# Kernel tuning notes

Measured on AMD Instinct MI355X. Metric: run time of the kernel, lower is better.

## Reference

```python
import itertools
import jax, jax.numpy as jnp
import numpy as np

N = 400000
CIN, COUT = 32, 64
K, STRIDE, PAD, DIL = 3, 2, 1, 1
SPATIAL = (200, 200, 16)
PRUNING_RATIO = 0.5

def _out_spatial():
    return tuple((s + 2 * PAD - DIL * (K - 1) - 1) // STRIDE + 1 for s in SPATIAL)


def setup_inputs() -> dict:
    key = jax.random.key(0)
    kf, kc0, kc1, kc2, kc3, km, kw = jax.random.split(key, 7)
    features = jax.random.normal(kf, (N, CIN), dtype=jnp.float32)
    b = jax.random.randint(kc0, (N,), 0, 2, dtype=jnp.int32)
    z = jax.random.randint(kc1, (N,), 0, SPATIAL[0], dtype=jnp.int32)
    y = jax.random.randint(kc2, (N,), 0, SPATIAL[1], dtype=jnp.int32)
    x = jax.random.randint(kc3, (N,), 0, SPATIAL[2], dtype=jnp.int32)
    coors = jnp.stack([b, z, y, x], axis=1)  # [N,4] = (batch, d0, d1, d2)
    mask = jax.random.uniform(km, (N,), dtype=jnp.float32)
    weight = jax.random.normal(kw, (K, K, K, CIN, COUT), dtype=jnp.float32) * 0.05
    return {"features": features, "coors": coors, "mask": mask, "weight": weight, "batch_size": 2}


def _sprs_conv(features, coors, mask, weight, batch_size):
    out_sp = _out_spatial()  # (100, 100, 8)
    num_out = batch_size * out_sp[0] * out_sp[1] * out_sp[2]
    n = features.shape[0]
    # rank-based pruning: keep top (1 - pruning_ratio) points as 'important'
    thr = jnp.sort(mask)[int(n * PRUNING_RATIO)]
    important = (mask >= thr)  # [N] bool

    b = coors[:, 0]
    pos = coors[:, 1:4]  # [N,3]
    out_sp_arr = jnp.array(out_sp, dtype=pos.dtype)

    # accumulators; slot num_out is a dump for invalid indices
    acc = jnp.zeros((num_out + 1, COUT), dtype=features.dtype)
    imp_cnt = jnp.zeros((num_out + 1,), dtype=jnp.int32)

    for off in itertools.product(range(K), repeat=3):
        off_arr = jnp.array(off, dtype=pos.dtype)
        num = pos + PAD - DIL * off_arr  # [N,3]
        oc = num // STRIDE
        valid = jnp.all(num % STRIDE == 0, axis=-1) & jnp.all(oc >= 0, axis=-1) & jnp.all(oc < out_sp_arr, axis=-1)
        lin = ((b * out_sp[0] + oc[:, 0]) * out_sp[1] + oc[:, 1]) * out_sp[2] + oc[:, 2]
        idx = jnp.where(valid, lin, num_out)
        vals = features @ weight[off[0], off[1], off[2]]  # [N,Cout] gather-GEMM
        acc = acc.at[idx].add(vals)  # scatter
        imp_cnt = imp_cnt.at[idx].add((important & valid).astype(jnp.int32))

    keep = (imp_cnt[:num_out] > 0)  # output positions reached by >=1 important point
    return acc[:num_out] * keep[:, None]


def reference(features, coors, mask, weight, batch_size):
    return _sprs_conv(features, coors, mask, weight, batch_size)
```

## Files before the change

kernel.cpp:

```cpp
#include <hip/hip_runtime.h>

#define CIN 32
#define COUT 64
#define OD0 100
#define OD1 100
#define OD2 8
#define IZ 200
#define IY 200
#define IX 16
#define NTAP 27
#define NCELLS (2 * IZ * IY * IX)
#define TOY 4
#define TOX 8
#define NROW 27
#define NCELL_R (NROW * 16)
#define CAPB 384


__global__ void hist0_fused_kernel(const float* __restrict__ mask, const int* __restrict__ coors,
                                   const float* __restrict__ W, int n,
                                   int* __restrict__ hist, int* __restrict__ S,
                                   float* __restrict__ Wt) {
    __shared__ int h[256];
    h[threadIdx.x] = 0;
    __syncthreads();
    for (int i = blockIdx.x * blockDim.x + threadIdx.x; i < n; i += gridDim.x * blockDim.x) {
        unsigned bits = __float_as_uint(mask[i]);
        atomicAdd(&h[bits >> 24], 1);
        const int4 c = ((const int4*)coors)[i];
        atomicAdd(&S[((c.x * IZ + c.y) * IY + c.z) * IX + c.w], 1);
    }
    for (int i = blockIdx.x * blockDim.x + threadIdx.x; i < NTAP * CIN * COUT;
         i += gridDim.x * blockDim.x) {
        int cout = i % COUT;
        int rest = i / COUT;
        int cin = rest % CIN;
        int tap = rest / CIN;
        Wt[((size_t)tap * COUT + cout) * CIN + cin] = W[i];
    }
    __syncthreads();
    int v = h[threadIdx.x];
    if (v) atomicAdd(&hist[threadIdx.x], v);
}


__global__ void hist8_kernel(const float* __restrict__ mask, int n, int level,
                             const int* __restrict__ state, int* __restrict__ hist) {
    __shared__ int h[256];
    h[threadIdx.x] = 0;
    __syncthreads();
    unsigned pfx = (unsigned)state[0];
    int sh = 24 - 8 * level;
    for (int i = blockIdx.x * blockDim.x + threadIdx.x; i < n; i += gridDim.x * blockDim.x) {
        unsigned bits = __float_as_uint(mask[i]);
        if ((bits >> (sh + 8)) == pfx)
            atomicAdd(&h[(bits >> sh) & 0xFF], 1);
    }
    __syncthreads();
    int v = h[threadIdx.x];
    if (v) atomicAdd(&hist[threadIdx.x], v);
}

__global__ void select8_kernel(const int* __restrict__ hist, int* __restrict__ state,
                               int level, int rankConst) {
    __shared__ int sc[256];
    sc[threadIdx.x] = hist[threadIdx.x];
    __syncthreads();
    if (threadIdx.x == 0) {
        int rank = level ? state[1] : rankConst;
        unsigned pfx = level ? (unsigned)state[0] : 0u;
        int c = 0;
        for (int j = 0; j < 256; j++) {
            int hv = sc[j];
            if (rank < c + hv) {
                state[0] = (int)((pfx << 8) | (unsigned)j);
                state[1] = rank - c;
                break;
            }
            c += hv;
        }
    }
}


__global__ void scan_l0_kernel(int* __restrict__ S, int* __restrict__ partials) {
    __shared__ int ts[256];
    int tid = threadIdx.x;
    int4 v = ((int4*)S)[blockIdx.x * 256 + tid];
    int s1 = v.x + v.y, s2 = s1 + v.z, s3 = s2 + v.w;
    ts[tid] = s3;
    __syncthreads();
    for (int off = 1; off < 256; off <<= 1) {
        int t = (tid >= off) ? ts[tid - off] : 0;
        __syncthreads();
        ts[tid] += t;
        __syncthreads();
    }
    int excl = ts[tid] - s3;
    int4 o;
    o.x = excl; o.y = excl + v.x; o.z = excl + s1; o.w = excl + s2;
    ((int4*)S)[blockIdx.x * 256 + tid] = o;
    if (tid == 255) partials[blockIdx.x] = ts[255];
}

__global__ void scan_l1_kernel(int* __restrict__ partials, int nP) {
    __shared__ int sums[256];
    int tid = threadIdx.x;
    int per = (nP + 255) / 256;
    int lo = tid * per, hi = lo + per;
    if (hi > nP) hi = nP;
    int s = 0;
    for (int j = lo; j < hi; j++) s += partials[j];
    sums[tid] = s;
    __syncthreads();
    for (int off = 1; off < 256; off <<= 1) {
        int t = (tid >= off) ? sums[tid - off] : 0;
        __syncthreads();
        sums[tid] += t;
        __syncthreads();
    }
    int run = sums[tid] - s;
    for (int j = lo; j < hi; j++) { int v = partials[j]; partials[j] = run; run += v; }
}

__global__ void scan_l2_kernel(int* __restrict__ S, const int* __restrict__ partials) {
    int add = partials[blockIdx.x];
    if (add == 0) return;
    int4 v = ((int4*)S)[blockIdx.x * 256 + threadIdx.x];
    v.x += add; v.y += add; v.z += add; v.w += add;
    ((int4*)S)[blockIdx.x * 256 + threadIdx.x] = v;
}

__global__ void scatter_points_kernel(const int* __restrict__ coors, const float* __restrict__ mask,
                                      const int* __restrict__ state, int n,
                                      int* __restrict__ S, int* __restrict__ entries) {
    int i = blockIdx.x * blockDim.x + threadIdx.x;
    if (i >= n) return;
    const int4 c = ((const int4*)coors)[i];
    int cell = ((c.x * IZ + c.y) * IY + c.z) * IX + c.w;
    float thr = __uint_as_float((unsigned)state[0]);
    int imp = (mask[i] >= thr) ? 1 : 0;
    int pos = atomicAdd(&S[cell], 1);
    entries[pos] = (i << 1) | imp;
}


__global__ void __launch_bounds__(256)
conv_kernel(const float* __restrict__ feat, const float* __restrict__ Wt,
            const int* __restrict__ S, const int* __restrict__ entries,
            float* __restrict__ out) {
    __shared__ float accS[TOY * TOX][COUT];
    __shared__ int   keepS[TOY * TOX];
    __shared__ int   sLds[NROW][17];
    __shared__ unsigned work[6][CAPB];
    __shared__ int   cnt[6];
    __shared__ int   notDone;

    int tid = threadIdx.x;
    int w = tid >> 6;
    int lane = tid & 63;

    int tile = blockIdx.x;
    int oyT = (tile % (OD1 / TOY)) * TOY;
    int rest = tile / (OD1 / TOY);
    int oz = rest % OD0;
    int bb = rest / OD0;

    {
        float4 z = make_float4(0.f, 0.f, 0.f, 0.f);
        float4* a4 = (float4*)&accS[0][0];
        a4[tid] = z;
        a4[tid + 256] = z;
        if (tid < TOY * TOX) keepS[tid] = 0;
    }

    for (int idx = tid; idx < NROW * 17; idx += 256) {
        int row = idx / 17, j = idx % 17;
        int plane = row / 9, pyL = row % 9;
        int pz = 2 * oz - 1 + plane;
        int py = 2 * oyT - 1 + pyL;
        int v = 0;
        if (pz >= 0 && py >= 0) {
            int cellFlat = ((bb * IZ + pz) * IY + py) * IX + (j - 1);
            if (cellFlat >= 0) v = S[cellFlat];
        }
        sLds[row][j] = v;
    }
    __syncthreads();

    int myCl[2]; int nMy = 0;
    for (int cl = tid; cl < NCELL_R; cl += 256) myCl[nMy++] = cl;
    int ci = 0;
    int pi = -1;

    for (;;) {
        if (tid < 6) cnt[tid] = 0;
        if (tid == 0) notDone = 0;
        __syncthreads();

        while (ci < nMy) {
            int cl = myCl[ci];
            int row = cl >> 4, px = cl & 15;
            int rs = (pi < 0) ? sLds[row][px] : pi;
            int re = sLds[row][px + 1];
            int plane = row / 9, pyL = row % 9;
            int bin = plane * 2 + (pyL & 1);
            bool blocked = false;
            for (int i = rs; i < re; i++) {
                int pos = atomicAdd(&cnt[bin], 1);
                if (pos >= CAPB) { pi = i; blocked = true; break; }
                int e = entries[i];
                work[bin][pos] = ((unsigned)(e >> 1) << 9) | (unsigned)((e & 1) << 8)
                               | (unsigned)(pyL << 4) | (unsigned)px;
            }
            if (blocked) break;
            ci++; pi = -1;
        }
        if (ci < nMy) notDone = 1;
        __syncthreads();

        for (int t = w; t < NTAP; t += 4) {
            int o0 = t / 9, r9 = t % 9, o1 = r9 / 3, o2 = r9 % 3;
            int bin = o0 * 2 + (o1 & 1);
            int nb = cnt[bin];
            if (nb > CAPB) nb = CAPB;
            if (nb == 0) continue;

            const float4* wp = (const float4*)(Wt + ((size_t)t * COUT + lane) * CIN);
            float4 w0 = wp[0], w1 = wp[1], w2 = wp[2], w3 = wp[3];
            float4 w4 = wp[4], w5 = wp[5], w6 = wp[6], w7 = wp[7];

            int pcl = -1;
            float4 f0, f1, f2, f3, f4, f5, f6, f7;

            for (int j = 0; j < nb; j++) {
                unsigned e = work[bin][j];
                int pyL = (int)((e >> 4) & 15u);
                int px  = (int)(e & 15u);
                int yy = (pyL - o1) >> 1;
                if ((unsigned)yy >= (unsigned)TOY) continue;
                int dx = px + 1 - o2;
                if (dx & 1) continue;
                int ox = dx >> 1;
                if ((unsigned)ox >= (unsigned)TOX) continue;

                int pid = (int)(e >> 9);
                const float4* fp = (const float4*)(feat + (size_t)pid * CIN);
                float4 n0 = fp[0], n1 = fp[1], n2 = fp[2], n3 = fp[3];
                float4 n4 = fp[4], n5 = fp[5], n6 = fp[6], n7 = fp[7];

                if (pcl >= 0) {
                    float a0 = 0.f, a1 = 0.f, a2 = 0.f, a3 = 0.f;
                    a0 = fmaf(f0.x, w0.x, a0); a0 = fmaf(f0.y, w0.y, a0);
                    a0 = fmaf(f0.z, w0.z, a0); a0 = fmaf(f0.w, w0.w, a0);
                    a1 = fmaf(f1.x, w1.x, a1); a1 = fmaf(f1.y, w1.y, a1);
                    a1 = fmaf(f1.z, w1.z, a1); a1 = fmaf(f1.w, w1.w, a1);
                    a2 = fmaf(f2.x, w2.x, a2); a2 = fmaf(f2.y, w2.y, a2);
                    a2 = fmaf(f2.z, w2.z, a2); a2 = fmaf(f2.w, w2.w, a2);
                    a3 = fmaf(f3.x, w3.x, a3); a3 = fmaf(f3.y, w3.y, a3);
                    a3 = fmaf(f3.z, w3.z, a3); a3 = fmaf(f3.w, w3.w, a3);
                    a0 = fmaf(f4.x, w4.x, a0); a0 = fmaf(f4.y, w4.y, a0);
                    a0 = fmaf(f4.z, w4.z, a0); a0 = fmaf(f4.w, w4.w, a0);
                    a1 = fmaf(f5.x, w5.x, a1); a1 = fmaf(f5.y, w5.y, a1);
                    a1 = fmaf(f5.z, w5.z, a1); a1 = fmaf(f5.w, w5.w, a1);
                    a2 = fmaf(f6.x, w6.x, a2); a2 = fmaf(f6.y, w6.y, a2);
                    a2 = fmaf(f6.z, w6.z, a2); a2 = fmaf(f6.w, w6.w, a2);
                    a3 = fmaf(f7.x, w7.x, a3); a3 = fmaf(f7.y, w7.y, a3);
                    a3 = fmaf(f7.z, w7.z, a3); a3 = fmaf(f7.w, w7.w, a3);
                    atomicAdd(&accS[pcl][lane], (a0 + a1) + (a2 + a3));
                }

                f0 = n0; f1 = n1; f2 = n2; f3 = n3;
                f4 = n4; f5 = n5; f6 = n6; f7 = n7;
                pcl = yy * TOX + ox;
                if (lane == 0 && (e & 0x100u)) keepS[pcl] = 1;
            }

            if (pcl >= 0) {
                float a0 = 0.f, a1 = 0.f, a2 = 0.f, a3 = 0.f;
                a0 = fmaf(f0.x, w0.x, a0); a0 = fmaf(f0.y, w0.y, a0);
                a0 = fmaf(f0.z, w0.z, a0); a0 = fmaf(f0.w, w0.w, a0);
                a1 = fmaf(f1.x, w1.x, a1); a1 = fmaf(f1.y, w1.y, a1);
                a1 = fmaf(f1.z, w1.z, a1); a1 = fmaf(f1.w, w1.w, a1);
                a2 = fmaf(f2.x, w2.x, a2); a2 = fmaf(f2.y, w2.y, a2);
                a2 = fmaf(f2.z, w2.z, a2); a2 = fmaf(f2.w, w2.w, a2);
                a3 = fmaf(f3.x, w3.x, a3); a3 = fmaf(f3.y, w3.y, a3);
                a3 = fmaf(f3.z, w3.z, a3); a3 = fmaf(f3.w, w3.w, a3);
                a0 = fmaf(f4.x, w4.x, a0); a0 = fmaf(f4.y, w4.y, a0);
                a0 = fmaf(f4.z, w4.z, a0); a0 = fmaf(f4.w, w4.w, a0);
                a1 = fmaf(f5.x, w5.x, a1); a1 = fmaf(f5.y, w5.y, a1);
                a1 = fmaf(f5.z, w5.z, a1); a1 = fmaf(f5.w, w5.w, a1);
                a2 = fmaf(f6.x, w6.x, a2); a2 = fmaf(f6.y, w6.y, a2);
                a2 = fmaf(f6.z, w6.z, a2); a2 = fmaf(f6.w, w6.w, a2);
                a3 = fmaf(f7.x, w7.x, a3); a3 = fmaf(f7.y, w7.y, a3);
                a3 = fmaf(f7.z, w7.z, a3); a3 = fmaf(f7.w, w7.w, a3);
                atomicAdd(&accS[pcl][lane], (a0 + a1) + (a2 + a3));
            }
        }
        __syncthreads();
        if (!notDone) break;
    }

#pragma unroll
    for (int k = 0; k < 8; k++) {
        int cl = w * 8 + k;
        int oy = oyT + (cl >> 3);
        int ox = cl & 7;
        size_t cellG = (((size_t)bb * OD0 + oz) * OD1 + oy) * OD2 + ox;
        out[cellG * COUT + lane] = keepS[cl] ? accS[cl][lane] : 0.f;
    }
}


__global__ void hist0_simple_kernel(const float* __restrict__ mask, int n, int* __restrict__ hist) {
    __shared__ int h[256];
    h[threadIdx.x] = 0;
    __syncthreads();
    for (int i = blockIdx.x * blockDim.x + threadIdx.x; i < n; i += gridDim.x * blockDim.x) {
        unsigned bits = __float_as_uint(mask[i]);
        atomicAdd(&h[bits >> 24], 1);
    }
    __syncthreads();
    int v = h[threadIdx.x];
    if (v) atomicAdd(&hist[threadIdx.x], v);
}

__global__ void __launch_bounds__(256)
scatter_kernel(const float* __restrict__ feat, const int* __restrict__ coors,
               const float* __restrict__ mask, const float* __restrict__ W,
               const int* __restrict__ state, float* __restrict__ out,
               int* __restrict__ keep, int n) {
    int gid = blockIdx.x * blockDim.x + threadIdx.x;
    int wave = gid >> 6;
    int lane = threadIdx.x & 63;
    if (wave >= n) return;

    const int4 c4 = ((const int4*)coors)[wave];
    int bb = c4.x, pz = c4.y, py = c4.z, px = c4.w;

    float thr = __uint_as_float((unsigned)state[0]);
    bool imp = mask[wave] >= thr;

    int oz[2], ozo[2], nz = 0;
    int oy[2], oyo[2], ny = 0;
    int ox[2], oxo[2], nx = 0;
#pragma unroll
    for (int o = 0; o < 3; o++) {
        int num = pz + 1 - o;
        if (num >= 0 && !(num & 1) && (num >> 1) < OD0) { oz[nz] = num >> 1; ozo[nz] = o; nz++; }
        num = py + 1 - o;
        if (num >= 0 && !(num & 1) && (num >> 1) < OD1) { oy[ny] = num >> 1; oyo[ny] = o; ny++; }
        num = px + 1 - o;
        if (num >= 0 && !(num & 1) && (num >> 1) < OD2) { ox[nx] = num >> 1; oxo[nx] = o; nx++; }
    }

    float f[CIN];
    const float4* fp = (const float4*)(feat + (size_t)wave * CIN);
#pragma unroll
    for (int j = 0; j < CIN / 4; j++) {
        float4 v = fp[j];
        f[4 * j + 0] = v.x; f[4 * j + 1] = v.y; f[4 * j + 2] = v.z; f[4 * j + 3] = v.w;
    }

    for (int a = 0; a < nz; a++)
        for (int b = 0; b < ny; b++)
            for (int c = 0; c < nx; c++) {
                int woff = ((ozo[a] * 3 + oyo[b]) * 3 + oxo[c]) * (CIN * COUT);
                const float* wcol = W + woff + lane;
                float acc = 0.f;
#pragma unroll
                for (int k = 0; k < CIN; k++) acc = fmaf(f[k], wcol[k * COUT], acc);
                int lin = ((bb * OD0 + oz[a]) * OD1 + oy[b]) * OD2 + ox[c];
                atomicAdd(out + (size_t)lin * COUT + lane, acc);
                if (imp && lane == 0) keep[lin] = 1;
            }
}

__global__ void finalize_kernel(float* __restrict__ out, const int* __restrict__ keep, int numOut) {
    int t = blockIdx.x * blockDim.x + threadIdx.x;
    if (t >= numOut * (COUT / 4)) return;
    int o = t >> 4;
    if (!keep[o]) ((float4*)out)[t] = make_float4(0.f, 0.f, 0.f, 0.f);
}


extern "C" void kernel_launch(void* const* d_in, const int* in_sizes, int n_in,
                              void* d_out, int out_size, void* d_ws, size_t ws_size,
                              hipStream_t stream) {
    const float* feat  = (const float*)d_in[0];
    const int*   coors = (const int*)d_in[1];
    const float* mask  = (const float*)d_in[2];
    const float* W     = (const float*)d_in[3];

    int n = in_sizes[2];
    int numOut = out_size / COUT;
    int rank = (int)(n * 0.5);

    const int blk = 256;
    int gN = (n + blk - 1) / blk;

    char* ws = (char*)d_ws;

    size_t offHist    = 0;
    size_t offState   = 4 * 256 * 4;
    size_t offS       = offState + 64;
    size_t offPart    = offS + (size_t)NCELLS * 4;
    size_t offEntries = offPart + 1280 * 4;
    size_t offWt      = offEntries + (size_t)n * 4;
    size_t need       = offWt + (size_t)NTAP * CIN * COUT * 4;

    int* hist  = (int*)(ws + offHist);
    int* state = (int*)(ws + offState);

    if (ws_size >= need) {
        int*   S       = (int*)(ws + offS);
        int*   part    = (int*)(ws + offPart);
        int*   entries = (int*)(ws + offEntries);
        float* Wt      = (float*)(ws + offWt);

        hipMemsetAsync(ws, 0, offS + (size_t)NCELLS * 4, stream);

        hist0_fused_kernel<<<256, blk, 0, stream>>>(mask, coors, W, n, hist, S, Wt);
        select8_kernel<<<1, 256, 0, stream>>>(hist, state, 0, rank);
        for (int lvl = 1; lvl < 4; lvl++) {
            hist8_kernel<<<256, blk, 0, stream>>>(mask, n, lvl, state, hist + lvl * 256);
            select8_kernel<<<1, 256, 0, stream>>>(hist + lvl * 256, state, lvl, rank);
        }

        int nBlocksScan = NCELLS / 1024;
        scan_l0_kernel<<<nBlocksScan, 256, 0, stream>>>(S, part);
        scan_l1_kernel<<<1, 256, 0, stream>>>(part, nBlocksScan);
        scan_l2_kernel<<<nBlocksScan, 256, 0, stream>>>(S, part);
        scatter_points_kernel<<<gN, blk, 0, stream>>>(coors, mask, state, n, S, entries);

        int nTiles = numOut / (TOY * TOX);
        conv_kernel<<<nTiles, 256, 0, stream>>>(feat, Wt, S, entries, (float*)d_out);
    } else {
        int* keep = (int*)(ws + offS);
        hipMemsetAsync(d_out, 0, (size_t)out_size * sizeof(float), stream);
        hipMemsetAsync(ws, 0, offS + (size_t)numOut * 4, stream);

        hist0_simple_kernel<<<256, blk, 0, stream>>>(mask, n, hist);
        select8_kernel<<<1, 256, 0, stream>>>(hist, state, 0, rank);
        for (int lvl = 1; lvl < 4; lvl++) {
            hist8_kernel<<<256, blk, 0, stream>>>(mask, n, lvl, state, hist + lvl * 256);
            select8_kernel<<<1, 256, 0, stream>>>(hist + lvl * 256, state, lvl, rank);
        }

        long long threads = (long long)n * 64;
        int gScatter = (int)((threads + blk - 1) / blk);
        scatter_kernel<<<gScatter, blk, 0, stream>>>(feat, coors, mask, W, state,
                                                     (float*)d_out, keep, n);

        int fin = numOut * (COUT / 4);
        finalize_kernel<<<(fin + blk - 1) / blk, blk, 0, stream>>>((float*)d_out, keep, numOut);
    }
}
```

Baseline: 733.6 us.

## Use two-pass 16-bit radix select and widen conv blocks to 512 threads

The top-k threshold search drops from four 8-bit histogram and select rounds to two 16-bit rounds, which removes several small serial kernel launches. The first histogram now goes straight to global atomics on a 65536-bin table instead of a shared-memory histogram. Separately, the conv kernel runs with 512 threads (8 waves) per tile, so each thread loads at most one cell and taps are spread over 8 waves, with an extra barrier to compute the done flag. Global atomic contention in the high histogram and a larger memset may offset the savings.

```diff
diff --git a/kernel.cpp b/kernel.cpp
--- a/kernel.cpp
+++ b/kernel.cpp
@@ -19,14 +19,11 @@
 
 __global__ void hist0_fused_kernel(const float* __restrict__ mask, const int* __restrict__ coors,
                                    const float* __restrict__ W, int n,
-                                   int* __restrict__ hist, int* __restrict__ S,
+                                   int* __restrict__ histHi, int* __restrict__ S,
                                    float* __restrict__ Wt) {
-    __shared__ int h[256];
-    h[threadIdx.x] = 0;
-    __syncthreads();
     for (int i = blockIdx.x * blockDim.x + threadIdx.x; i < n; i += gridDim.x * blockDim.x) {
         unsigned bits = __float_as_uint(mask[i]);
-        atomicAdd(&h[bits >> 24], 1);
+        atomicAdd(&histHi[bits >> 16], 1);
         const int4 c = ((const int4*)coors)[i];
         atomicAdd(&S[((c.x * IZ + c.y) * IY + c.z) * IX + c.w], 1);
     }
@@ -38,43 +35,74 @@
         int tap = rest / CIN;
         Wt[((size_t)tap * COUT + cout) * CIN + cin] = W[i];
     }
-    __syncthreads();
-    int v = h[threadIdx.x];
-    if (v) atomicAdd(&hist[threadIdx.x], v);
-}
-
-
-__global__ void hist8_kernel(const float* __restrict__ mask, int n, int level,
-                             const int* __restrict__ state, int* __restrict__ hist) {
-    __shared__ int h[256];
-    h[threadIdx.x] = 0;
-    __syncthreads();
-    unsigned pfx = (unsigned)state[0];
-    int sh = 24 - 8 * level;
-    for (int i = blockIdx.x * blockDim.x + threadIdx.x; i < n; i += gridDim.x * blockDim.x) {
-        unsigned bits = __float_as_uint(mask[i]);
-        if ((bits >> (sh + 8)) == pfx)
-            atomicAdd(&h[(bits >> sh) & 0xFF], 1);
-    }
-    __syncthreads();
-    int v = h[threadIdx.x];
-    if (v) atomicAdd(&hist[threadIdx.x], v);
-}
-
-__global__ void select8_kernel(const int* __restrict__ hist, int* __restrict__ state,
-                               int level, int rankConst) {
-    __shared__ int sc[256];
-    sc[threadIdx.x] = hist[threadIdx.x];
-    __syncthreads();
-    if (threadIdx.x == 0) {
-        int rank = level ? state[1] : rankConst;
-        unsigned pfx = level ? (unsigned)state[0] : 0u;
+}
+
+__global__ void hist_hi_simple_kernel(const float* __restrict__ mask, int n, int* __restrict__ hist) {
+    int i = blockIdx.x * blockDim.x + threadIdx.x;
+    if (i >= n) return;
+    unsigned bits = __float_as_uint(mask[i]);
+    atomicAdd(&hist[bits >> 16], 1);
+}
+
+__global__ void select16_kernel(const int* __restrict__ hist, const int* rankSrc,
+                                int rankConst, int* __restrict__ outPair) {
+    __shared__ int partial[256];
+    __shared__ int scan[257];
+    int t = threadIdx.x;
+    int rank = rankSrc ? *rankSrc : rankConst;
+    const int* h = hist + t * 256;
+    int sum = 0;
+    for (int j = 0; j < 256; j++) sum += h[j];
+    partial[t] = sum;
+    __syncthreads();
+    if (t == 0) {
         int c = 0;
+        for (int j = 0; j < 256; j++) { scan[j] = c; c += partial[j]; }
+        scan[256] = c;
+    }
+    __syncthreads();
+    int base = scan[t];
+    if (rank >= base && rank < scan[t + 1]) {
+        int c = base;
         for (int j = 0; j < 256; j++) {
-            int hv = sc[j];
+            int hv = h[j];
+            if (rank < c + hv) { outPair[0] = t * 256 + j; outPair[1] = rank - c; break; }
+            c += hv;
+        }
+    }
+}
+
+__global__ void hist_lo_kernel(const float* __restrict__ mask, int n,
+                               const int* __restrict__ state, int* __restrict__ hist) {
+    int i = blockIdx.x * blockDim.x + threadIdx.x;
+    if (i >= n) return;
+    unsigned bits = __float_as_uint(mask[i]);
+    if ((int)(bits >> 16) == state[2]) atomicAdd(&hist[bits & 0xFFFFu], 1);
+}
+
+__global__ void selectLo_kernel(const int* __restrict__ hist, int* __restrict__ state) {
+    __shared__ int partial[256];
+    __shared__ int scan[257];
+    int t = threadIdx.x;
+    int rank = state[3];
+    const int* h = hist + t * 256;
+    int sum = 0;
+    for (int j = 0; j < 256; j++) sum += h[j];
+    partial[t] = sum;
+    __syncthreads();
+    if (t == 0) {
+        int c = 0;
+        for (int j = 0; j < 256; j++) { scan[j] = c; c += partial[j]; }
+        scan[256] = c;
+    }
+    __syncthreads();
+    int base = scan[t];
+    if (rank >= base && rank < scan[t + 1]) {
+        int c = base;
+        for (int j = 0; j < 256; j++) {
+            int hv = h[j];
             if (rank < c + hv) {
-                state[0] = (int)((pfx << 8) | (unsigned)j);
-                state[1] = rank - c;
+                state[0] = (state[2] << 16) | (t * 256 + j);
                 break;
             }
             c += hv;
@@ -145,7 +173,7 @@
 }
 
 
-__global__ void __launch_bounds__(256)
+__global__ void __launch_bounds__(512, 6)
 conv_kernel(const float* __restrict__ feat, const float* __restrict__ Wt,
             const int* __restrict__ S, const int* __restrict__ entries,
             float* __restrict__ out) {
@@ -168,13 +196,11 @@
 
     {
         float4 z = make_float4(0.f, 0.f, 0.f, 0.f);
-        float4* a4 = (float4*)&accS[0][0];
-        a4[tid] = z;
-        a4[tid + 256] = z;
+        ((float4*)&accS[0][0])[tid] = z;
         if (tid < TOY * TOX) keepS[tid] = 0;
     }
 
-    for (int idx = tid; idx < NROW * 17; idx += 256) {
+    for (int idx = tid; idx < NROW * 17; idx += 512) {
         int row = idx / 17, j = idx % 17;
         int plane = row / 9, pyL = row % 9;
         int pz = 2 * oz - 1 + plane;
@@ -188,9 +214,7 @@
     }
     __syncthreads();
 
-    int myCl[2]; int nMy = 0;
-    for (int cl = tid; cl < NCELL_R; cl += 256) myCl[nMy++] = cl;
-    int ci = 0;
+    int myCell = (tid < NCELL_R) ? tid : -1;
     int pi = -1;
 
     for (;;) {
@@ -198,9 +222,8 @@
         if (tid == 0) notDone = 0;
         __syncthreads();
 
-        while (ci < nMy) {
-            int cl = myCl[ci];
-            int row = cl >> 4, px = cl & 15;
+        if (myCell >= 0) {
+            int row = myCell >> 4, px = myCell & 15;
             int rs = (pi < 0) ? sLds[row][px] : pi;
             int re = sLds[row][px + 1];
             int plane = row / 9, pyL = row % 9;
@@ -213,13 +236,16 @@
                 work[bin][pos] = ((unsigned)(e >> 1) << 9) | (unsigned)((e & 1) << 8)
                                | (unsigned)(pyL << 4) | (unsigned)px;
             }
-            if (blocked) break;
-            ci++; pi = -1;
+            if (!blocked) myCell = -1;
         }
-        if (ci < nMy) notDone = 1;
-        __syncthreads();
-
-        for (int t = w; t < NTAP; t += 4) {
+        __syncthreads();
+        if (tid == 0) notDone = 0;
+        __syncthreads();
+        if (myCell >= 0) notDone = 1;
+        __syncthreads();
+        int more = notDone;
+
+        for (int t = w; t < NTAP; t += 8) {
             int o0 = t / 9, r9 = t % 9, o1 = r9 / 3, o2 = r9 % 3;
             int bin = o0 * 2 + (o1 & 1);
             int nb = cnt[bin];
@@ -298,12 +324,12 @@
             }
         }
         __syncthreads();
-        if (!notDone) break;
+        if (!more) break;
     }
 
 #pragma unroll
-    for (int k = 0; k < 8; k++) {
-        int cl = w * 8 + k;
+    for (int k = 0; k < 4; k++) {
+        int cl = w * 4 + k;
         int oy = oyT + (cl >> 3);
         int ox = cl & 7;
         size_t cellG = (((size_t)bb * OD0 + oz) * OD1 + oy) * OD2 + ox;
@@ -311,19 +337,6 @@
     }
 }
 
-
-__global__ void hist0_simple_kernel(const float* __restrict__ mask, int n, int* __restrict__ hist) {
-    __shared__ int h[256];
-    h[threadIdx.x] = 0;
-    __syncthreads();
-    for (int i = blockIdx.x * blockDim.x + threadIdx.x; i < n; i += gridDim.x * blockDim.x) {
-        unsigned bits = __float_as_uint(mask[i]);
-        atomicAdd(&h[bits >> 24], 1);
-    }
-    __syncthreads();
-    int v = h[threadIdx.x];
-    if (v) atomicAdd(&hist[threadIdx.x], v);
-}
 
 __global__ void __launch_bounds__(256)
 scatter_kernel(const float* __restrict__ feat, const int* __restrict__ coors,
@@ -401,16 +414,18 @@
 
     char* ws = (char*)d_ws;
 
-    size_t offHist    = 0;
-    size_t offState   = 4 * 256 * 4;
+    size_t offHistHi  = 0;
+    size_t offHistLo  = 65536 * 4;
+    size_t offState   = 2 * 65536 * 4;
     size_t offS       = offState + 64;
     size_t offPart    = offS + (size_t)NCELLS * 4;
     size_t offEntries = offPart + 1280 * 4;
     size_t offWt      = offEntries + (size_t)n * 4;
     size_t need       = offWt + (size_t)NTAP * CIN * COUT * 4;
 
-    int* hist  = (int*)(ws + offHist);
-    int* state = (int*)(ws + offState);
+    int* histHi = (int*)(ws + offHistHi);
+    int* histLo = (int*)(ws + offHistLo);
+    int* state  = (int*)(ws + offState);
 
     if (ws_size >= need) {
         int*   S       = (int*)(ws + offS);
@@ -420,12 +435,10 @@
 
         hipMemsetAsync(ws, 0, offS + (size_t)NCELLS * 4, stream);
 
-        hist0_fused_kernel<<<256, blk, 0, stream>>>(mask, coors, W, n, hist, S, Wt);
-        select8_kernel<<<1, 256, 0, stream>>>(hist, state, 0, rank);
-        for (int lvl = 1; lvl < 4; lvl++) {
-            hist8_kernel<<<256, blk, 0, stream>>>(mask, n, lvl, state, hist + lvl * 256);
-            select8_kernel<<<1, 256, 0, stream>>>(hist + lvl * 256, state, lvl, rank);
-        }
+        hist0_fused_kernel<<<256, blk, 0, stream>>>(mask, coors, W, n, histHi, S, Wt);
+        select16_kernel<<<1, 256, 0, stream>>>(histHi, nullptr, rank, state + 2);
+        hist_lo_kernel<<<gN, blk, 0, stream>>>(mask, n, state, histLo);
+        selectLo_kernel<<<1, 256, 0, stream>>>(histLo, state);
 
         int nBlocksScan = NCELLS / 1024;
         scan_l0_kernel<<<nBlocksScan, 256, 0, stream>>>(S, part);
@@ -434,18 +447,16 @@
         scatter_points_kernel<<<gN, blk, 0, stream>>>(coors, mask, state, n, S, entries);
 
         int nTiles = numOut / (TOY * TOX);
-        conv_kernel<<<nTiles, 256, 0, stream>>>(feat, Wt, S, entries, (float*)d_out);
+        conv_kernel<<<nTiles, 512, 0, stream>>>(feat, Wt, S, entries, (float*)d_out);
     } else {
         int* keep = (int*)(ws + offS);
         hipMemsetAsync(d_out, 0, (size_t)out_size * sizeof(float), stream);
         hipMemsetAsync(ws, 0, offS + (size_t)numOut * 4, stream);
 
-        hist0_simple_kernel<<<256, blk, 0, stream>>>(mask, n, hist);
-        select8_kernel<<<1, 256, 0, stream>>>(hist, state, 0, rank);
-        for (int lvl = 1; lvl < 4; lvl++) {
-            hist8_kernel<<<256, blk, 0, stream>>>(mask, n, lvl, state, hist + lvl * 256);
-            select8_kernel<<<1, 256, 0, stream>>>(hist + lvl * 256, state, lvl, rank);
-        }
+        hist_hi_simple_kernel<<<gN, blk, 0, stream>>>(mask, n, histHi);
+        select16_kernel<<<1, 256, 0, stream>>>(histHi, nullptr, rank, state + 2);
+        hist_lo_kernel<<<gN, blk, 0, stream>>>(mask, n, state, histLo);
+        selectLo_kernel<<<1, 256, 0, stream>>>(histLo, state);
 
         long long threads = (long long)n * 64;
         int gScatter = (int)((threads + blk - 1) / blk);
```

New measurement: 2.019 ms. 2.75x slower.
